# Optimization experiments

Measured on AMD Instinct MI355X. Metric: run time of the kernel, lower is better.

The kernel has to match this reference:

```python
import jax, jax.numpy as jnp
import numpy as np

EPS = 1e-5

def _batchnorm_train(x, gamma, beta):
    # training-mode BN over (N, H, W) per channel, biased variance (as torch)
    mean = jnp.mean(x, axis=(0, 2, 3), keepdims=True)
    var = jnp.mean(jnp.square(x - mean), axis=(0, 2, 3), keepdims=True)
    xn = (x - mean) * jax.lax.rsqrt(var + EPS)
    return xn * gamma[None, :, None, None] + beta[None, :, None, None]

def setup_inputs() -> dict:
    key = jax.random.key(0)
    k1, k2 = jax.random.split(key)
    x = jax.random.normal(k1, (32, 128, 128, 128), dtype=jnp.float32)  # [B,C,H,W]
    conv_w = jax.random.normal(k2, (1, 2, 7, 7), dtype=jnp.float32) * 0.1  # OIHW
    return {
        "x": x,
        "conv_w": conv_w,
        "bn1_gamma": jnp.ones((2,), jnp.float32),
        "bn1_beta": jnp.zeros((2,), jnp.float32),
        "bn2_gamma": jnp.ones((1,), jnp.float32),
        "bn2_beta": jnp.zeros((1,), jnp.float32),
    }

def reference(x, conv_w, bn1_gamma, bn1_beta, bn2_gamma, bn2_beta):
    avg_feat = jnp.mean(x, axis=1, keepdims=True)   # [B,1,H,W]
    max_feat = jnp.max(x, axis=1, keepdims=True)    # [B,1,H,W]
    feat = jnp.concatenate([avg_feat, max_feat], axis=1)  # [B,2,H,W]
    feat = _batchnorm_train(feat, bn1_gamma, bn1_beta)
    feat = jax.lax.conv_general_dilated(
        feat, conv_w,
        window_strides=(1, 1),
        padding=[(3, 3), (3, 3)],
        dimension_numbers=("NCHW", "OIHW", "NCHW"),
    )  # [B,1,H,W]
    feat = _batchnorm_train(feat, bn2_gamma, bn2_beta)
    attention = jax.nn.sigmoid(feat)
    return attention * x
```

## Files before the change

### kernel.cpp

```cpp
#include <hip/hip_runtime.h>
#include <math.h>

#define B_    32
#define C_    128
#define HW_   16384
#define NPIX  524288
#define EPSF  1e-5f

typedef float vfloat4 __attribute__((ext_vector_type(4)));

__device__ __forceinline__ float wave_sum(float v) {
#pragma unroll
    for (int off = 32; off > 0; off >>= 1) v += __shfl_down(v, off, 64);
    return v;
}

__global__ __launch_bounds__(256) void k_reduce(const float* __restrict__ x,
                                                float* __restrict__ feat,
                                                float* __restrict__ stats) {
    int lane = threadIdx.x & 63, wid = threadIdx.x >> 6;
    int pg   = (blockIdx.x * 4 + wid) * 32 + (lane & 31);
    int b    = pg >> 12;
    int hw   = (pg & 4095) << 2;
    int ch0  = (lane >> 5) * 64;

    const float4* xp = reinterpret_cast<const float4*>(
        x + (size_t)b * C_ * HW_ + (size_t)ch0 * HW_ + hw);
    float4 s = make_float4(0.f, 0.f, 0.f, 0.f);
    float4 m = make_float4(-INFINITY, -INFINITY, -INFINITY, -INFINITY);
#pragma unroll 8
    for (int c = 0; c < 64; ++c) {
        float4 v = xp[(size_t)c * (HW_ / 4)];
        s.x += v.x; s.y += v.y; s.z += v.z; s.w += v.w;
        m.x = fmaxf(m.x, v.x); m.y = fmaxf(m.y, v.y);
        m.z = fmaxf(m.z, v.z); m.w = fmaxf(m.w, v.w);
    }
    s.x += __shfl_xor(s.x, 32, 64); s.y += __shfl_xor(s.y, 32, 64);
    s.z += __shfl_xor(s.z, 32, 64); s.w += __shfl_xor(s.w, 32, 64);
    m.x = fmaxf(m.x, __shfl_xor(m.x, 32, 64)); m.y = fmaxf(m.y, __shfl_xor(m.y, 32, 64));
    m.z = fmaxf(m.z, __shfl_xor(m.z, 32, 64)); m.w = fmaxf(m.w, __shfl_xor(m.w, 32, 64));

    const float inv = 1.0f / 128.0f;
    float4 a = make_float4(s.x * inv, s.y * inv, s.z * inv, s.w * inv);
    float* fb = feat + (size_t)b * 2 * HW_ + hw;
    if (lane < 32) *reinterpret_cast<float4*>(fb)       = a;
    else           *reinterpret_cast<float4*>(fb + HW_) = m;

    float vals[4];
    vals[0] = a.x + a.y + a.z + a.w;
    vals[1] = a.x*a.x + a.y*a.y + a.z*a.z + a.w*a.w;
    vals[2] = m.x + m.y + m.z + m.w;
    vals[3] = m.x*m.x + m.y*m.y + m.z*m.z + m.w*m.w;

    __shared__ float red[4];
#pragma unroll
    for (int i = 0; i < 4; ++i) {
        float v = wave_sum(vals[i]);
        if (lane == 0) red[wid] = v;
        __syncthreads();
        if (threadIdx.x == 0)
            atomicAdd(stats + i, 0.5f * (red[0] + red[1] + red[2] + red[3]));
        __syncthreads();
    }
}

__global__ __launch_bounds__(256) void k_conv(const float* __restrict__ feat,
                                              const float* __restrict__ cw,
                                              const float* __restrict__ g1,
                                              const float* __restrict__ be1,
                                              float* __restrict__ convout,
                                              float* __restrict__ stats) {
    __shared__ float w_s[98];
    __shared__ float sc_s[2], sh_s[2];
    if (threadIdx.x < 98) w_s[threadIdx.x] = cw[threadIdx.x];
    if (threadIdx.x < 2) {
        const float invn = 1.0f / (float)NPIX;
        int c = threadIdx.x;
        float mean = stats[2 * c] * invn;
        float var  = stats[2 * c + 1] * invn - mean * mean;
        float sc   = g1[c] / sqrtf(var + EPSF);
        sc_s[c] = sc;
        sh_s[c] = be1[c] - mean * sc;
    }
    __syncthreads();

    int t  = blockIdx.x * 256 + threadIdx.x;
    int b  = t >> 12;
    int pg = t & 4095;
    int h  = pg >> 5;
    int w4 = (pg & 31) << 2;
    const float* fb = feat + (size_t)b * 2 * HW_;

    float acc0 = 0.f, acc1 = 0.f, acc2 = 0.f, acc3 = 0.f;
#pragma unroll
    for (int c = 0; c < 2; ++c) {
        float sc = sc_s[c], sh = sh_s[c];
        const float* fc = fb + c * HW_;
#pragma unroll
        for (int kh = 0; kh < 7; ++kh) {
            int hh = h + kh - 3;
            if ((unsigned)hh >= 128u) continue;
            const float* row = fc + hh * 128;
            float v[10];
#pragma unroll
            for (int i = 0; i < 10; ++i) {
                int ww = w4 - 3 + i;
                v[i] = ((unsigned)ww < 128u) ? row[ww] * sc + sh : 0.f;
            }
#pragma unroll
            for (int kw = 0; kw < 7; ++kw) {
                float wt = w_s[c * 49 + kh * 7 + kw];
                acc0 += v[kw]     * wt;
                acc1 += v[kw + 1] * wt;
                acc2 += v[kw + 2] * wt;
                acc3 += v[kw + 3] * wt;
            }
        }
    }
    *reinterpret_cast<float4*>(convout + (size_t)b * HW_ + h * 128 + w4) =
        make_float4(acc0, acc1, acc2, acc3);

    __shared__ float red[4];
    int lane = threadIdx.x & 63, wid = threadIdx.x >> 6;
    float v = wave_sum(acc0 + acc1 + acc2 + acc3);
    if (lane == 0) red[wid] = v;
    __syncthreads();
    if (threadIdx.x == 0) atomicAdd(stats + 4, red[0] + red[1] + red[2] + red[3]);
    __syncthreads();
    v = wave_sum(acc0*acc0 + acc1*acc1 + acc2*acc2 + acc3*acc3);
    if (lane == 0) red[wid] = v;
    __syncthreads();
    if (threadIdx.x == 0) atomicAdd(stats + 5, red[0] + red[1] + red[2] + red[3]);
}

__global__ __launch_bounds__(256) void k_apply(const float* __restrict__ x,
                                               const float* __restrict__ convout,
                                               const float* __restrict__ g2,
                                               const float* __restrict__ be2,
                                               const float* __restrict__ stats,
                                               float* __restrict__ out) {
    int t  = (gridDim.x - 1 - blockIdx.x) * 256 + threadIdx.x;
    int hw = (t & 4095) << 2;
    int c  = (t >> 12) & 127;
    int b  = t >> 19;

    const float invn = 1.0f / (float)NPIX;
    float mean = stats[4] * invn;
    float var  = stats[5] * invn - mean * mean;
    float s    = g2[0] / sqrtf(var + EPSF);
    float sh   = be2[0] - mean * s;

    float4 cv = *reinterpret_cast<const float4*>(convout + b * HW_ + hw);
    float4 att;
    att.x = 1.f / (1.f + __expf(-(cv.x * s + sh)));
    att.y = 1.f / (1.f + __expf(-(cv.y * s + sh)));
    att.z = 1.f / (1.f + __expf(-(cv.z * s + sh)));
    att.w = 1.f / (1.f + __expf(-(cv.w * s + sh)));

    size_t xi = ((size_t)(b * 128 + c)) * HW_ + hw;
    float4 xv = *reinterpret_cast<const float4*>(x + xi);
    vfloat4 o = { xv.x * att.x, xv.y * att.y, xv.z * att.z, xv.w * att.w };
    __builtin_nontemporal_store(o, reinterpret_cast<vfloat4*>(out + xi));
}

extern "C" void kernel_launch(void* const* d_in, const int* in_sizes, int n_in,
                              void* d_out, int out_size, void* d_ws, size_t ws_size,
                              hipStream_t stream) {
    const float* x  = (const float*)d_in[0];
    const float* cw = (const float*)d_in[1];
    const float* g1 = (const float*)d_in[2];
    const float* b1 = (const float*)d_in[3];
    const float* g2 = (const float*)d_in[4];
    const float* b2 = (const float*)d_in[5];
    float* out = (float*)d_out;

    char* ws = (char*)d_ws;
    float* feat    = (float*)ws;
    float* convout = (float*)(ws + 4u * 1024 * 1024);
    float* stats   = (float*)(ws + 6u * 1024 * 1024);

    (void)hipMemsetAsync(stats, 0, 8 * sizeof(float), stream);
    k_reduce<<<1024,  256, 0, stream>>>(x, feat, stats);
    k_conv  <<<512,   256, 0, stream>>>(feat, cw, g1, b1, convout, stats);
    k_apply <<<65536, 256, 0, stream>>>(x, convout, g2, b2, stats, out);
}
```

Measured before the change: 194.5 us.

## Replace BN1 atomics with per-block partials, drop memset, process two channels per thread

Stage-1 statistics are now written as per-block partial sums and reduced in every conv block, rather than accumulated with atomics. The BN2 accumulators are zeroed inside k_reduce, which removes the separate memset launch. k_apply now handles two channels per thread with nontemporal loads, so each thread computes the sigmoid for two output channels and the grid is halved. In exchange, each conv block re-reads 4K partials, and correctness depends on ordering: k_reduce's zeroing must finish before k_conv's atomics, which stream ordering guarantees.

```diff
diff --git a/kernel.cpp b/kernel.cpp
--- a/kernel.cpp
+++ b/kernel.cpp
@@ -17,7 +17,10 @@
 
 __global__ __launch_bounds__(256) void k_reduce(const float* __restrict__ x,
                                                 float* __restrict__ feat,
-                                                float* __restrict__ stats) {
+                                                float* __restrict__ pp,
+                                                float* __restrict__ bn2) {
+    if (blockIdx.x == 0 && threadIdx.x < 2) bn2[threadIdx.x] = 0.f;
+
     int lane = threadIdx.x & 63, wid = threadIdx.x >> 6;
     int pg   = (blockIdx.x * 4 + wid) * 32 + (lane & 31);
     int b    = pg >> 12;
@@ -59,7 +62,7 @@
         if (lane == 0) red[wid] = v;
         __syncthreads();
         if (threadIdx.x == 0)
-            atomicAdd(stats + i, 0.5f * (red[0] + red[1] + red[2] + red[3]));
+            pp[i * 1024 + blockIdx.x] = 0.5f * (red[0] + red[1] + red[2] + red[3]);
         __syncthreads();
     }
 }
@@ -68,16 +71,30 @@
                                               const float* __restrict__ cw,
                                               const float* __restrict__ g1,
                                               const float* __restrict__ be1,
+                                              const float* __restrict__ pp,
                                               float* __restrict__ convout,
-                                              float* __restrict__ stats) {
+                                              float* __restrict__ bn2) {
     __shared__ float w_s[98];
     __shared__ float sc_s[2], sh_s[2];
+    __shared__ float red4[4][4];
+    int lane = threadIdx.x & 63, wid = threadIdx.x >> 6;
+
     if (threadIdx.x < 98) w_s[threadIdx.x] = cw[threadIdx.x];
+#pragma unroll
+    for (int i = 0; i < 4; ++i) {
+        const float* p = pp + i * 1024 + threadIdx.x;
+        float a = p[0] + p[256] + p[512] + p[768];
+        a = wave_sum(a);
+        if (lane == 0) red4[i][wid] = a;
+    }
+    __syncthreads();
     if (threadIdx.x < 2) {
         const float invn = 1.0f / (float)NPIX;
         int c = threadIdx.x;
-        float mean = stats[2 * c] * invn;
-        float var  = stats[2 * c + 1] * invn - mean * mean;
+        float S = red4[2*c][0] + red4[2*c][1] + red4[2*c][2] + red4[2*c][3];
+        float Q = red4[2*c+1][0] + red4[2*c+1][1] + red4[2*c+1][2] + red4[2*c+1][3];
+        float mean = S * invn;
+        float var  = Q * invn - mean * mean;
         float sc   = g1[c] / sqrtf(var + EPSF);
         sc_s[c] = sc;
         sh_s[c] = be1[c] - mean * sc;
@@ -121,46 +138,48 @@
         make_float4(acc0, acc1, acc2, acc3);
 
     __shared__ float red[4];
-    int lane = threadIdx.x & 63, wid = threadIdx.x >> 6;
     float v = wave_sum(acc0 + acc1 + acc2 + acc3);
     if (lane == 0) red[wid] = v;
     __syncthreads();
-    if (threadIdx.x == 0) atomicAdd(stats + 4, red[0] + red[1] + red[2] + red[3]);
+    if (threadIdx.x == 0) atomicAdd(bn2 + 0, red[0] + red[1] + red[2] + red[3]);
     __syncthreads();
     v = wave_sum(acc0*acc0 + acc1*acc1 + acc2*acc2 + acc3*acc3);
     if (lane == 0) red[wid] = v;
     __syncthreads();
-    if (threadIdx.x == 0) atomicAdd(stats + 5, red[0] + red[1] + red[2] + red[3]);
+    if (threadIdx.x == 0) atomicAdd(bn2 + 1, red[0] + red[1] + red[2] + red[3]);
 }
 
 __global__ __launch_bounds__(256) void k_apply(const float* __restrict__ x,
                                                const float* __restrict__ convout,
                                                const float* __restrict__ g2,
                                                const float* __restrict__ be2,
-                                               const float* __restrict__ stats,
+                                               const float* __restrict__ bn2,
                                                float* __restrict__ out) {
-    int t  = (gridDim.x - 1 - blockIdx.x) * 256 + threadIdx.x;
-    int hw = (t & 4095) << 2;
-    int c  = (t >> 12) & 127;
-    int b  = t >> 19;
+    int t   = (gridDim.x - 1 - blockIdx.x) * 256 + threadIdx.x;
+    int hw  = (t & 4095) << 2;
+    int clo = (t >> 12) & 63;
+    int b   = t >> 18;
 
     const float invn = 1.0f / (float)NPIX;
-    float mean = stats[4] * invn;
-    float var  = stats[5] * invn - mean * mean;
+    float mean = bn2[0] * invn;
+    float var  = bn2[1] * invn - mean * mean;
     float s    = g2[0] / sqrtf(var + EPSF);
     float sh   = be2[0] - mean * s;
 
-    float4 cv = *reinterpret_cast<const float4*>(convout + b * HW_ + hw);
-    float4 att;
-    att.x = 1.f / (1.f + __expf(-(cv.x * s + sh)));
-    att.y = 1.f / (1.f + __expf(-(cv.y * s + sh)));
-    att.z = 1.f / (1.f + __expf(-(cv.z * s + sh)));
-    att.w = 1.f / (1.f + __expf(-(cv.w * s + sh)));
-
-    size_t xi = ((size_t)(b * 128 + c)) * HW_ + hw;
-    float4 xv = *reinterpret_cast<const float4*>(x + xi);
-    vfloat4 o = { xv.x * att.x, xv.y * att.y, xv.z * att.z, xv.w * att.w };
-    __builtin_nontemporal_store(o, reinterpret_cast<vfloat4*>(out + xi));
+    float4 cv = *reinterpret_cast<const float4*>(convout + (size_t)b * HW_ + hw);
+    float att0 = 1.f / (1.f + __expf(-(cv.x * s + sh)));
+    float att1 = 1.f / (1.f + __expf(-(cv.y * s + sh)));
+    float att2 = 1.f / (1.f + __expf(-(cv.z * s + sh)));
+    float att3 = 1.f / (1.f + __expf(-(cv.w * s + sh)));
+
+    size_t xi0 = ((size_t)(b * 128 + clo)) * HW_ + hw;
+    size_t xi1 = xi0 + (size_t)64 * HW_;
+    vfloat4 x0 = __builtin_nontemporal_load(reinterpret_cast<const vfloat4*>(x + xi0));
+    vfloat4 x1 = __builtin_nontemporal_load(reinterpret_cast<const vfloat4*>(x + xi1));
+    vfloat4 o0 = { x0.x * att0, x0.y * att1, x0.z * att2, x0.w * att3 };
+    vfloat4 o1 = { x1.x * att0, x1.y * att1, x1.z * att2, x1.w * att3 };
+    __builtin_nontemporal_store(o0, reinterpret_cast<vfloat4*>(out + xi0));
+    __builtin_nontemporal_store(o1, reinterpret_cast<vfloat4*>(out + xi1));
 }
 
 extern "C" void kernel_launch(void* const* d_in, const int* in_sizes, int n_in,
@@ -177,10 +196,10 @@
     char* ws = (char*)d_ws;
     float* feat    = (float*)ws;
     float* convout = (float*)(ws + 4u * 1024 * 1024);
-    float* stats   = (float*)(ws + 6u * 1024 * 1024);
-
-    (void)hipMemsetAsync(stats, 0, 8 * sizeof(float), stream);
-    k_reduce<<<1024,  256, 0, stream>>>(x, feat, stats);
-    k_conv  <<<512,   256, 0, stream>>>(feat, cw, g1, b1, convout, stats);
-    k_apply <<<65536, 256, 0, stream>>>(x, convout, g2, b2, stats, out);
-}
+    float* pp      = (float*)(ws + 6u * 1024 * 1024);
+    float* bn2     = (float*)(ws + 6u * 1024 * 1024 + 65536);
+
+    k_reduce<<<1024,  256, 0, stream>>>(x, feat, pp, bn2);
+    k_conv  <<<512,   256, 0, stream>>>(feat, cw, g1, b1, pp, convout, bn2);
+    k_apply <<<32768, 256, 0, stream>>>(x, convout, g2, b2, bn2, out);
+}
```

New measurement: 170.3 us. -12.5%, faster.
